# Kernel tuning notes

Hardware: AMD Instinct MI355X
Metric: run time of the kernel (lower is better)

## Reference

```python
import jax, jax.numpy as jnp
import numpy as np
import math

DIM = 2048
NUM_HEADS = 16
HEAD_DIM = 128
SEQ = 2048
BATCH = 2
THETA = 10000.0


def _rope_freqs(seq_len, head_dim, theta=THETA):
    half = head_dim // 2
    inv = 1.0 / (theta ** (np.arange(0, half, dtype=np.float32) / half))
    t = np.arange(seq_len, dtype=np.float32)
    ang = np.outer(t, inv)  # [S, half]
    return jnp.asarray(np.cos(ang)), jnp.asarray(np.sin(ang))


def setup_inputs() -> dict:
    key = jax.random.key(0)
    ks = jax.random.split(key, 5)
    s = 1.0 / math.sqrt(DIM)
    cos, sin = _rope_freqs(SEQ, HEAD_DIM)
    return {
        "x": jax.random.normal(ks[0], (BATCH, SEQ, DIM), dtype=jnp.float32),
        "wq": jax.random.normal(ks[1], (DIM, NUM_HEADS * HEAD_DIM), dtype=jnp.float32) * s,
        "wk": jax.random.normal(ks[2], (DIM, NUM_HEADS * HEAD_DIM), dtype=jnp.float32) * s,
        "wv": jax.random.normal(ks[3], (DIM, NUM_HEADS * HEAD_DIM), dtype=jnp.float32) * s,
        "wo": jax.random.normal(ks[4], (NUM_HEADS * HEAD_DIM, DIM), dtype=jnp.float32) * s,
        "freqs_cos": cos,
        "freqs_sin": sin,
    }


def _apply_rope(x, cos, sin):
    # x: [B, S, H, Hd]; cos/sin: [S, Hd//2]
    B, S, H, Hd = x.shape
    xr = x.astype(jnp.float32).reshape(B, S, H, Hd // 2, 2)
    x0, x1 = xr[..., 0], xr[..., 1]
    c = cos[:S][None, :, None, :]
    sn = sin[:S][None, :, None, :]
    o0 = x0 * c - x1 * sn
    o1 = x0 * sn + x1 * c
    return jnp.stack([o0, o1], axis=-1).reshape(B, S, H, Hd)


def reference(x, wq, wk, wv, wo, freqs_cos, freqs_sin):
    B, S, D = x.shape
    H, Hd = NUM_HEADS, HEAD_DIM
    q = (x @ wq).reshape(B, S, H, Hd)
    k = (x @ wk).reshape(B, S, H, Hd)
    v = (x @ wv).reshape(B, S, H, Hd)
    q = _apply_rope(q, freqs_cos, freqs_sin)
    k = _apply_rope(k, freqs_cos, freqs_sin)
    # [B, H, S, S] causal attention scores
    scores = jnp.einsum("bqhd,bkhd->bhqk", q, k) / math.sqrt(Hd)
    causal = jnp.tril(jnp.ones((S, S), dtype=bool))
    scores = jnp.where(causal[None, None], scores, -jnp.inf)
    probs = jax.nn.softmax(scores.astype(jnp.float32), axis=-1)
    o = jnp.einsum("bhqk,bkhd->bqhd", probs, v).reshape(B, S, H * Hd)
    return o @ wo
```

## Files before the change

### kernel.cpp

```cpp
#include <hip/hip_runtime.h>
#include <hip/hip_bf16.h>

typedef __bf16 bf16;
typedef __attribute__((ext_vector_type(8))) __bf16 bf16x8;
typedef __attribute__((ext_vector_type(4))) __bf16 bf16x4;
typedef __attribute__((ext_vector_type(4))) float  f32x4;

typedef const void __attribute__((address_space(1)))* gas_t;
typedef void __attribute__((address_space(3)))* las_t;

__device__ __forceinline__ void gload16(const void* g, void* l) {
  __builtin_amdgcn_global_load_lds((gas_t)g, (las_t)l, 16, 0, 0);
}
__device__ __forceinline__ f32x4 mfma16(bf16x8 a, bf16x8 b, f32x4 c) {
  return __builtin_amdgcn_mfma_f32_16x16x32_bf16(a, b, c, 0, 0, 0);
}
#define BARRIER() do { asm volatile("" ::: "memory"); \
  __builtin_amdgcn_s_barrier(); asm volatile("" ::: "memory"); } while (0)

constexpr int SEQL = 2048;
constexpr int DM   = 2048;
constexpr int HD   = 128;
constexpr int MR   = 4096;

__global__ __launch_bounds__(256) void cvt_x(const float* __restrict__ x,
                                             bf16* __restrict__ xb) {
  const size_t i = ((size_t)blockIdx.x * 256 + threadIdx.x) * 4;
  const f32x4 v = *reinterpret_cast<const f32x4*>(x + i);
  bf16x4 o;
  #pragma unroll
  for (int j = 0; j < 4; ++j) o[j] = (bf16)v[j];
  *reinterpret_cast<bf16x4*>(xb + i) = o;
}

__global__ __launch_bounds__(256) void transpose_w(
    const float* __restrict__ w0, const float* __restrict__ w1,
    const float* __restrict__ w2, const float* __restrict__ w3,
    bf16* __restrict__ wqkvt, bf16* __restrict__ wot) {
  const int z = blockIdx.z;
  const float* src = (z == 0) ? w0 : (z == 1) ? w1 : (z == 2) ? w2 : w3;
  bf16* dst = (z < 3) ? (wqkvt + (size_t)z * DM * DM) : wot;
  __shared__ float tile[32][33];
  const int tx = threadIdx.x, ty = threadIdx.y;
  const int x0 = blockIdx.x * 32, y0 = blockIdx.y * 32;
  #pragma unroll
  for (int i = 0; i < 4; ++i)
    tile[ty + 8 * i][tx] = src[(size_t)(y0 + ty + 8 * i) * DM + x0 + tx];
  __syncthreads();
  #pragma unroll
  for (int i = 0; i < 4; ++i)
    dst[(size_t)(x0 + ty + 8 * i) * DM + y0 + tx] = (bf16)tile[tx][ty + 8 * i];
}

__global__ __launch_bounds__(256) void rope_k(bf16* __restrict__ Q,
                                              bf16* __restrict__ Kk,
                                              const float* __restrict__ fc,
                                              const float* __restrict__ fs) {
  bf16* X = blockIdx.y ? Kk : Q;
  const size_t tid = (size_t)blockIdx.x * 256 + threadIdx.x;
  const size_t e0 = tid * 8;
  const int col = (int)(e0 & (DM - 1));
  const int row = (int)(e0 >> 11);
  const int s   = row & (SEQL - 1);
  const int p0  = (col & (HD - 1)) >> 1;
  bf16x8 v = *reinterpret_cast<bf16x8*>(X + e0);
  const f32x4 c  = *reinterpret_cast<const f32x4*>(fc + (size_t)s * 64 + p0);
  const f32x4 sn = *reinterpret_cast<const f32x4*>(fs + (size_t)s * 64 + p0);
  #pragma unroll
  for (int j = 0; j < 4; ++j) {
    const float x0 = (float)v[2 * j], x1 = (float)v[2 * j + 1];
    v[2 * j]     = (bf16)(x0 * c[j] - x1 * sn[j]);
    v[2 * j + 1] = (bf16)(x0 * sn[j] + x1 * c[j]);
  }
  *reinterpret_cast<bf16x8*>(X + e0) = v;
}

#define LDA4(DST, BASE, ROWOFF)                                                \
  {                                                                            \
    const char* ap_ = (BASE) + ((ROWOFF) + lo) * 128;                          \
    DST[0] = *(const bf16x8*)(ap_ + su0);                                      \
    DST[1] = *(const bf16x8*)(ap_ + su1);                                      \
    DST[2] = *(const bf16x8*)(ap_ + 2048 + su0);                               \
    DST[3] = *(const bf16x8*)(ap_ + 2048 + su1);                               \
  }
#define MFMAQ(Q, AR)                                                           \
  {                                                                            \
    __builtin_amdgcn_s_setprio(1);                                             \
    _Pragma("unroll")                                                          \
    for (int nf = 0; nf < 4; ++nf) {                                           \
      acc[2 * (Q)][nf]     = mfma16(AR[0], bfr[nf][0], acc[2 * (Q)][nf]);      \
      acc[2 * (Q)][nf]     = mfma16(AR[1], bfr[nf][1], acc[2 * (Q)][nf]);      \
      acc[2 * (Q) + 1][nf] = mfma16(AR[2], bfr[nf][0], acc[2 * (Q) + 1][nf]);  \
      acc[2 * (Q) + 1][nf] = mfma16(AR[3], bfr[nf][1], acc[2 * (Q) + 1][nf]);  \
    }                                                                          \
    __builtin_amdgcn_s_setprio(0);                                             \
  }

__global__ __launch_bounds__(512, 2) void gemm8(
    const bf16* __restrict__ A, const bf16* __restrict__ Bt,
    bf16* __restrict__ Cb, const int M, const int N, const int K) {
  __shared__ __attribute__((aligned(16))) char lds[131072];
  const int t = threadIdx.x;
  const int wid = t >> 6, lane = t & 63, lo = lane & 15, hi = lane >> 4;
  const int wm = wid >> 2, wn = wid & 3;

  const int bid = blockIdx.x;
  const int xcd = bid & 7, idx = bid >> 3;
  const int my = (xcd << 1) | (idx & 1);
  const int nxz = idx >> 1;
  const int nx = nxz & 7, z = nxz >> 3;
  const int m0 = my * 256, n0 = nx * 256;
  const bf16* Bt_ = Bt + (size_t)z * N * K;
  bf16* Cb_ = Cb + (size_t)z * M * N;

  const int urow  = (wid << 3) + (lane >> 3);
  const int uunit = (lane & 7) ^ ((lane >> 3) & 7);
  const bf16* gA = A   + (size_t)(m0 + urow) * K + uunit * 8;
  const bf16* gB = Bt_ + (size_t)(n0 + urow) * K + uunit * 8;
  char* lw = lds + wid * 1024;
  const int NT = K >> 6;

  auto stg = [&](const bf16* gbase, int buf, int op, int h, int kt) {
    const bf16* g = gbase + (size_t)(h * 128) * K + kt * 64;
    char* l = lw + (((buf << 1) | op) * 2 + h) * 16384;
    gload16(g, l);
    gload16(g + (size_t)64 * K, l + 8192);
  };
  auto stB0 = [&](int k2) { stg(gB, k2 & 1, 1, 0, k2); };
  auto stB1 = [&](int k2) { stg(gB, k2 & 1, 1, 1, k2); };
  auto stA0 = [&](int k2) { stg(gA, k2 & 1, 0, 0, k2); };
  auto stA1 = [&](int k2) { stg(gA, k2 & 1, 0, 1, k2); };

  f32x4 acc[8][4];
  #pragma unroll
  for (int i = 0; i < 8; ++i)
    #pragma unroll
    for (int j = 0; j < 4; ++j) acc[i][j] = (f32x4){0.f, 0.f, 0.f, 0.f};

  const int su0 = (hi ^ (lo & 7)) * 16;
  const int su1 = ((4 + hi) ^ (lo & 7)) * 16;

  stB0(0); stB1(0); stA0(0); stA1(0);
  stB0(1); stB1(1); stA0(1); stA1(1);
  asm volatile("s_waitcnt vmcnt(8)" ::: "memory");
  BARRIER();

  bf16x8 aP0[4], aP1[4];
  LDA4(aP0, lds + wm * 16384, 0);

  #pragma unroll 1
  for (int kt = 0; kt < NT; ++kt) {
    const int bc = kt & 1;
    const char* aB = lds + (bc * 4 + wm) * 16384;
    const char* bB = lds + ((bc * 2 + 1) * 2 + (wn >> 1)) * 16384;
    const char* aN = lds + (((kt + 1) & 1) * 4 + wm) * 16384;
    bf16x8 bfr[4][2];
    {
      const char* bp = bB + ((wn & 1) * 64 + lo) * 128;
      #pragma unroll
      for (int nf = 0; nf < 4; ++nf) {
        bfr[nf][0] = *(const bf16x8*)(bp + nf * 2048 + su0);
        bfr[nf][1] = *(const bf16x8*)(bp + nf * 2048 + su1);
      }
    }
    LDA4(aP1, aB, 32);
    BARRIER();
    MFMAQ(0, aP0)
    BARRIER();
    LDA4(aP0, aB, 64);
    if (kt + 2 < NT) stB0(kt + 2);
    BARRIER();
    MFMAQ(1, aP1)
    BARRIER();
    LDA4(aP1, aB, 96);
    if (kt + 2 < NT) stB1(kt + 2);
    BARRIER();
    MFMAQ(2, aP0)
    BARRIER();
    if (kt + 2 < NT)      { asm volatile("s_waitcnt vmcnt(4)" ::: "memory"); }
    else if (kt + 1 < NT) { asm volatile("s_waitcnt vmcnt(0)" ::: "memory"); }
    BARRIER();
    if (kt + 1 < NT) LDA4(aP0, aN, 0);
    if (kt + 2 < NT) { stA0(kt + 2); stA1(kt + 2); }
    MFMAQ(3, aP1)
    BARRIER();
  }

  #pragma unroll
  for (int mf = 0; mf < 8; ++mf)
    #pragma unroll
    for (int nf = 0; nf < 4; ++nf)
      #pragma unroll
      for (int r = 0; r < 4; ++r) {
        const size_t row = m0 + wm * 128 + mf * 16 + hi * 4 + r;
        const size_t col = n0 + wn * 64 + nf * 16 + lo;
        Cb_[row * N + col] = (bf16)acc[mf][nf][r];
      }
}

__global__ __launch_bounds__(256) void gemm_bt_f32(
    const bf16* __restrict__ A, const bf16* __restrict__ Bt,
    float* __restrict__ Cf, const int M, const int N, const int K) {
  const int t = threadIdx.x;
  const int wid = t >> 6, lane = t & 63, lo = lane & 15, hi = lane >> 4;
  const int m0 = blockIdx.y * 128, n0 = blockIdx.x * 128;
  __shared__ bf16 As[128 * 32];
  __shared__ bf16 Bs[128 * 32];
  const int wr = wid >> 1, wc = wid & 1;
  const f32x4 zero4 = {0.f, 0.f, 0.f, 0.f};
  f32x4 acc[4][4];
  #pragma unroll
  for (int i = 0; i < 4; ++i)
    #pragma unroll
    for (int j = 0; j < 4; ++j) acc[i][j] = zero4;

  const int r_a = t >> 2;
  const int ul  = ((t & 3) ^ (r_a & 3)) * 8;
  const bf16* gA0 = A  + (size_t)(m0 + r_a) * K + ul;
  const bf16* gB0 = Bt + (size_t)(n0 + r_a) * K + ul;
  char* lA = (char*)As + wid * 1024;
  char* lB = (char*)Bs + wid * 1024;

  const int ru = (hi ^ (lo & 3)) * 8;

  for (int k0 = 0; k0 < K; k0 += 32) {
    gload16(gA0 + k0, lA);
    gload16(gA0 + (size_t)64 * K + k0, lA + 4096);
    gload16(gB0 + k0, lB);
    gload16(gB0 + (size_t)64 * K + k0, lB + 4096);
    __syncthreads();
    bf16x8 af[4], bb[4];
    #pragma unroll
    for (int i = 0; i < 4; ++i)
      af[i] = *reinterpret_cast<const bf16x8*>(As + (wr * 64 + i * 16 + lo) * 32 + ru);
    #pragma unroll
    for (int i = 0; i < 4; ++i)
      bb[i] = *reinterpret_cast<const bf16x8*>(Bs + (wc * 64 + i * 16 + lo) * 32 + ru);
    #pragma unroll
    for (int mi = 0; mi < 4; ++mi)
      #pragma unroll
      for (int ni = 0; ni < 4; ++ni)
        acc[mi][ni] = mfma16(af[mi], bb[ni], acc[mi][ni]);
    __syncthreads();
  }
  #pragma unroll
  for (int mi = 0; mi < 4; ++mi)
    #pragma unroll
    for (int ni = 0; ni < 4; ++ni)
      #pragma unroll
      for (int r = 0; r < 4; ++r) {
        const size_t row = m0 + wr * 64 + mi * 16 + hi * 4 + r;
        const size_t col = n0 + wc * 64 + ni * 16 + lo;
        Cf[row * N + col] = acc[mi][ni][r];
      }
}

__global__ __launch_bounds__(512) void flash_fwd(
    const bf16* __restrict__ Qg, const bf16* __restrict__ Kg,
    const bf16* __restrict__ Vg, bf16* __restrict__ Og) {
  const int t = threadIdx.x;
  const int wid = t >> 6, lane = t & 63, lo = lane & 15, hi = lane >> 4;
  const int h  = blockIdx.y;
  const int b  = blockIdx.z;

  __shared__ bf16 Ks[64 * 128];
  __shared__ bf16 Vt[128 * 64];
  __shared__ bf16 Ps[8][16 * 64];

  const size_t hoff = (size_t)b * SEQL * DM + (size_t)h * HD;
  const float SCALE_LOG2 = 0.12751743f;

  const int krow = t >> 4;
  const int kul  = ((t & 15) ^ (krow & 15)) * 8;
  const int vd0  = (t & 31) * 4;
  const int vg   = (t >> 5) & 15;
  char* myP = (char*)(Ps[wid]);
  const f32x4 zero4 = {0.f, 0.f, 0.f, 0.f};

  #pragma unroll 1
  for (int pass = 0; pass < 2; ++pass) {
    const int q0 = (pass ? (15 - (int)blockIdx.x) : (int)blockIdx.x) * 128;

    bf16x8 qf[4];
    {
      const bf16* qrow = Qg + hoff + (size_t)(q0 + wid * 16 + lo) * DM;
      #pragma unroll
      for (int kc = 0; kc < 4; ++kc)
        qf[kc] = *reinterpret_cast<const bf16x8*>(qrow + kc * 32 + hi * 8);
    }

    f32x4 acc[8];
    #pragma unroll
    for (int i = 0; i < 8; ++i) acc[i] = zero4;
    float m_run = -1e30f, l_run = 0.f;

    const int ntiles = q0 / 64 + 2;
    #pragma unroll 1
    for (int it = 0; it < ntiles; ++it) {
      const int kv0 = it * 64;
      {
        const bf16* gK = Kg + hoff + (size_t)(kv0 + krow) * DM + kul;
        char* lK = (char*)Ks + wid * 1024;
        gload16(gK, lK);
        gload16(gK + (size_t)32 * DM, lK + 8192);
      }
      {
        const bf16* gV = Vg + hoff + (size_t)(kv0 + vg * 4) * DM + vd0;
        bf16x4 ld[4];
        #pragma unroll
        for (int e = 0; e < 4; ++e)
          ld[e] = *reinterpret_cast<const bf16x4*>(gV + (size_t)e * DM);
        #pragma unroll
        for (int c = 0; c < 4; ++c) {
          const int d = vd0 + c;
          const int sw = (d ^ (d >> 3)) & 7;
          bf16x4 w;
          #pragma unroll
          for (int e = 0; e < 4; ++e) w[e] = ld[e][c];
          *reinterpret_cast<bf16x4*>(Vt + d * 64 + (((vg >> 1) ^ sw) * 8) +
                                     (vg & 1) * 4) = w;
        }
      }
      __syncthreads();

      f32x4 s[4];
      #pragma unroll
      for (int nf = 0; nf < 4; ++nf) s[nf] = zero4;
      #pragma unroll
      for (int nf = 0; nf < 4; ++nf) {
        const bf16* krp = Ks + (nf * 16 + lo) * 128;
        #pragma unroll
        for (int kc = 0; kc < 4; ++kc) {
          const bf16x8 kb = *reinterpret_cast<const bf16x8*>(krp + (((kc * 4 + hi) ^ lo) * 8));
          s[nf] = mfma16(kb, qf[kc], s[nf]);
        }
      }
      const bool boundary = (kv0 + 63 > q0 + wid * 16);
      #pragma unroll
      for (int nf = 0; nf < 4; ++nf)
        #pragma unroll
        for (int r = 0; r < 4; ++r) {
          float v = s[nf][r] * SCALE_LOG2;
          if (boundary && (kv0 + nf * 16 + hi * 4 + r > q0 + wid * 16 + lo)) v = -1e30f;
          s[nf][r] = v;
        }
      float pmax = -1e30f;
      #pragma unroll
      for (int nf = 0; nf < 4; ++nf)
        #pragma unroll
        for (int r = 0; r < 4; ++r) pmax = fmaxf(pmax, s[nf][r]);
      pmax = fmaxf(pmax, __shfl_xor(pmax, 16, 64));
      pmax = fmaxf(pmax, __shfl_xor(pmax, 32, 64));
      float mnew = m_run;
      if (!__all(pmax <= m_run)) {
        mnew = fmaxf(m_run, pmax);
        const float fctr = exp2f(m_run - mnew);
        m_run = mnew;
        l_run *= fctr;
        float fa[4];
        #pragma unroll
        for (int r = 0; r < 4; ++r) fa[r] = __shfl(fctr, hi * 4 + r, 64);
        #pragma unroll
        for (int i = 0; i < 8; ++i)
          #pragma unroll
          for (int r = 0; r < 4; ++r) acc[i][r] *= fa[r];
      }
      float sum = 0.f;
      #pragma unroll
      for (int nf = 0; nf < 4; ++nf)
        #pragma unroll
        for (int r = 0; r < 4; ++r) {
          const float p = exp2f(s[nf][r] - mnew);
          s[nf][r] = p;
          sum += p;
        }
      sum += __shfl_xor(sum, 16, 64);
      sum += __shfl_xor(sum, 32, 64);
      l_run += sum;
      #pragma unroll
      for (int nf = 0; nf < 4; ++nf) {
        bf16x4 w;
        #pragma unroll
        for (int r = 0; r < 4; ++r) w[r] = (bf16)s[nf][r];
        *reinterpret_cast<bf16x4*>(myP + lo * 128 +
            (((nf * 2 + (hi >> 1)) ^ (lo & 7)) * 16) + (hi & 1) * 8) = w;
      }
      bf16x8 pa[2];
      #pragma unroll
      for (int kc = 0; kc < 2; ++kc)
        pa[kc] = *reinterpret_cast<const bf16x8*>(myP + lo * 128 +
            (((kc * 4 + hi) ^ (lo & 7)) * 16));
      #pragma unroll
      for (int nf = 0; nf < 8; ++nf) {
        const int d = nf * 16 + lo;
        const int sw = (d ^ (d >> 3)) & 7;
        const bf16* vrp = Vt + d * 64;
        #pragma unroll
        for (int kc = 0; kc < 2; ++kc) {
          const bf16x8 bv = *reinterpret_cast<const bf16x8*>(vrp + (((kc * 4 + hi) ^ sw) * 8));
          acc[nf] = mfma16(pa[kc], bv, acc[nf]);
        }
      }
      __syncthreads();
    }

    const float linv = 1.f / l_run;
    float la[4];
    #pragma unroll
    for (int r = 0; r < 4; ++r) la[r] = __shfl(linv, hi * 4 + r, 64);
    #pragma unroll
    for (int nf = 0; nf < 8; ++nf)
      #pragma unroll
      for (int r = 0; r < 4; ++r) {
        const size_t row = q0 + wid * 16 + hi * 4 + r;
        Og[hoff + row * DM + nf * 16 + lo] = (bf16)(acc[nf][r] * la[r]);
      }
  }
}

extern "C" void kernel_launch(void* const* d_in, const int* in_sizes, int n_in,
                              void* d_out, int out_size, void* d_ws, size_t ws_size,
                              hipStream_t stream) {
  const float* x  = (const float*)d_in[0];
  const float* wq = (const float*)d_in[1];
  const float* wk = (const float*)d_in[2];
  const float* wv = (const float*)d_in[3];
  const float* wo = (const float*)d_in[4];
  const float* fc = (const float*)d_in[5];
  const float* fs = (const float*)d_in[6];
  float* out = (float*)d_out;

  char* ws = (char*)d_ws;
  bf16* xb    = (bf16*)ws;
  bf16* wqkvt = (bf16*)(ws + (16ull << 20));
  bf16* wot   = (bf16*)(ws + (40ull << 20));
  bf16* qkv   = (bf16*)(ws + (48ull << 20));
  bf16* Qb = qkv;
  bf16* Kb = qkv + (size_t)MR * DM;
  bf16* Vb = qkv + 2 * (size_t)MR * DM;

  cvt_x<<<8192, 256, 0, stream>>>(x, xb);
  transpose_w<<<dim3(64, 64, 4), dim3(32, 8), 0, stream>>>(wq, wk, wv, wo, wqkvt, wot);
  gemm8<<<384, 512, 0, stream>>>(xb, wqkvt, qkv, MR, DM, DM);
  rope_k<<<dim3(4096, 2), 256, 0, stream>>>(Qb, Kb, fc, fs);
  flash_fwd<<<dim3(8, 16, 2), 512, 0, stream>>>(Qb, Kb, Vb, xb );
  gemm_bt_f32<<<dim3(16, 32), 256, 0, stream>>>(xb, wot, out, MR, DM, DM);
}
```

Measured before the change: 419.0 us.

## Reuse pipelined GEMM for output projection and widen flash-attention per-wave query tile

Templates the pipelined 256x256 gemm8 kernel on output type so the output projection can use it with fp32 stores, replacing the simple single-buffered gemm_bt_f32. Flash attention now launches 256-thread blocks, each wave handling 32 query rows (two 16-row subtiles). Each K/V tile loaded into LDS is therefore reused across twice as many MFMAs per wave. The two-pass per-block load balancing is dropped in favour of reversing query-tile order by batch index. Risks include only 128 blocks for the output GEMM, which underfills the CUs, plus higher register pressure and less even causal work per block in attention.

```diff
diff --git a/kernel.cpp b/kernel.cpp
--- a/kernel.cpp
+++ b/kernel.cpp
@@ -96,9 +96,10 @@
     __builtin_amdgcn_s_setprio(0);                                             \
   }
 
+template <bool F32OUT>
 __global__ __launch_bounds__(512, 2) void gemm8(
     const bf16* __restrict__ A, const bf16* __restrict__ Bt,
-    bf16* __restrict__ Cb, const int M, const int N, const int K) {
+    void* __restrict__ Cv, const int M, const int N, const int K) {
   __shared__ __attribute__((aligned(16))) char lds[131072];
   const int t = threadIdx.x;
   const int wid = t >> 6, lane = t & 63, lo = lane & 15, hi = lane >> 4;
@@ -111,7 +112,6 @@
   const int nx = nxz & 7, z = nxz >> 3;
   const int m0 = my * 256, n0 = nx * 256;
   const bf16* Bt_ = Bt + (size_t)z * N * K;
-  bf16* Cb_ = Cb + (size_t)z * M * N;
 
   const int urow  = (wid << 3) + (lane >> 3);
   const int uunit = (lane & 7) ^ ((lane >> 3) & 7);
@@ -194,217 +194,176 @@
       for (int r = 0; r < 4; ++r) {
         const size_t row = m0 + wm * 128 + mf * 16 + hi * 4 + r;
         const size_t col = n0 + wn * 64 + nf * 16 + lo;
-        Cb_[row * N + col] = (bf16)acc[mf][nf][r];
-      }
-}
-
-__global__ __launch_bounds__(256) void gemm_bt_f32(
-    const bf16* __restrict__ A, const bf16* __restrict__ Bt,
-    float* __restrict__ Cf, const int M, const int N, const int K) {
-  const int t = threadIdx.x;
-  const int wid = t >> 6, lane = t & 63, lo = lane & 15, hi = lane >> 4;
-  const int m0 = blockIdx.y * 128, n0 = blockIdx.x * 128;
-  __shared__ bf16 As[128 * 32];
-  __shared__ bf16 Bs[128 * 32];
-  const int wr = wid >> 1, wc = wid & 1;
-  const f32x4 zero4 = {0.f, 0.f, 0.f, 0.f};
-  f32x4 acc[4][4];
-  #pragma unroll
-  for (int i = 0; i < 4; ++i)
-    #pragma unroll
-    for (int j = 0; j < 4; ++j) acc[i][j] = zero4;
-
-  const int r_a = t >> 2;
-  const int ul  = ((t & 3) ^ (r_a & 3)) * 8;
-  const bf16* gA0 = A  + (size_t)(m0 + r_a) * K + ul;
-  const bf16* gB0 = Bt + (size_t)(n0 + r_a) * K + ul;
-  char* lA = (char*)As + wid * 1024;
-  char* lB = (char*)Bs + wid * 1024;
-
-  const int ru = (hi ^ (lo & 3)) * 8;
-
-  for (int k0 = 0; k0 < K; k0 += 32) {
-    gload16(gA0 + k0, lA);
-    gload16(gA0 + (size_t)64 * K + k0, lA + 4096);
-    gload16(gB0 + k0, lB);
-    gload16(gB0 + (size_t)64 * K + k0, lB + 4096);
-    __syncthreads();
-    bf16x8 af[4], bb[4];
-    #pragma unroll
-    for (int i = 0; i < 4; ++i)
-      af[i] = *reinterpret_cast<const bf16x8*>(As + (wr * 64 + i * 16 + lo) * 32 + ru);
-    #pragma unroll
-    for (int i = 0; i < 4; ++i)
-      bb[i] = *reinterpret_cast<const bf16x8*>(Bs + (wc * 64 + i * 16 + lo) * 32 + ru);
-    #pragma unroll
-    for (int mi = 0; mi < 4; ++mi)
-      #pragma unroll
-      for (int ni = 0; ni < 4; ++ni)
-        acc[mi][ni] = mfma16(af[mi], bb[ni], acc[mi][ni]);
-    __syncthreads();
-  }
-  #pragma unroll
-  for (int mi = 0; mi < 4; ++mi)
-    #pragma unroll
-    for (int ni = 0; ni < 4; ++ni)
-      #pragma unroll
-      for (int r = 0; r < 4; ++r) {
-        const size_t row = m0 + wr * 64 + mi * 16 + hi * 4 + r;
-        const size_t col = n0 + wc * 64 + ni * 16 + lo;
-        Cf[row * N + col] = acc[mi][ni][r];
-      }
-}
-
-__global__ __launch_bounds__(512) void flash_fwd(
+        if (F32OUT)
+          ((float*)Cv)[((size_t)z * M * N) + row * N + col] = acc[mf][nf][r];
+        else
+          ((bf16*)Cv)[((size_t)z * M * N) + row * N + col] = (bf16)acc[mf][nf][r];
+      }
+}
+
+__global__ __launch_bounds__(256, 2) void flash_fwd(
     const bf16* __restrict__ Qg, const bf16* __restrict__ Kg,
     const bf16* __restrict__ Vg, bf16* __restrict__ Og) {
   const int t = threadIdx.x;
   const int wid = t >> 6, lane = t & 63, lo = lane & 15, hi = lane >> 4;
   const int h  = blockIdx.y;
   const int b  = blockIdx.z;
+  const int qi = b ? (15 - (int)blockIdx.x) : (int)blockIdx.x;
+  const int q0 = qi * 128;
 
   __shared__ bf16 Ks[64 * 128];
   __shared__ bf16 Vt[128 * 64];
-  __shared__ bf16 Ps[8][16 * 64];
+  __shared__ bf16 Ps[4][32 * 64];
 
   const size_t hoff = (size_t)b * SEQL * DM + (size_t)h * HD;
   const float SCALE_LOG2 = 0.12751743f;
 
   const int krow = t >> 4;
-  const int kul  = ((t & 15) ^ (krow & 15)) * 8;
+  const int kul  = ((t & 15) ^ krow) * 8;
   const int vd0  = (t & 31) * 4;
-  const int vg   = (t >> 5) & 15;
+  const int vg   = t >> 5;
   char* myP = (char*)(Ps[wid]);
   const f32x4 zero4 = {0.f, 0.f, 0.f, 0.f};
 
+  bf16x8 qf[2][4];
+  #pragma unroll
+  for (int s = 0; s < 2; ++s) {
+    const bf16* qrow = Qg + hoff + (size_t)(q0 + wid * 32 + s * 16 + lo) * DM;
+    #pragma unroll
+    for (int kc = 0; kc < 4; ++kc)
+      qf[s][kc] = *reinterpret_cast<const bf16x8*>(qrow + kc * 32 + hi * 8);
+  }
+
+  f32x4 acc[2][8];
+  #pragma unroll
+  for (int s = 0; s < 2; ++s)
+    #pragma unroll
+    for (int i = 0; i < 8; ++i) acc[s][i] = zero4;
+  float m_run[2] = {-1e30f, -1e30f}, l_run[2] = {0.f, 0.f};
+
+  const int ntiles = q0 / 64 + 2;
   #pragma unroll 1
-  for (int pass = 0; pass < 2; ++pass) {
-    const int q0 = (pass ? (15 - (int)blockIdx.x) : (int)blockIdx.x) * 128;
-
-    bf16x8 qf[4];
+  for (int it = 0; it < ntiles; ++it) {
+    const int kv0 = it * 64;
     {
-      const bf16* qrow = Qg + hoff + (size_t)(q0 + wid * 16 + lo) * DM;
-      #pragma unroll
-      for (int kc = 0; kc < 4; ++kc)
-        qf[kc] = *reinterpret_cast<const bf16x8*>(qrow + kc * 32 + hi * 8);
-    }
-
-    f32x4 acc[8];
-    #pragma unroll
-    for (int i = 0; i < 8; ++i) acc[i] = zero4;
-    float m_run = -1e30f, l_run = 0.f;
-
-    const int ntiles = q0 / 64 + 2;
-    #pragma unroll 1
-    for (int it = 0; it < ntiles; ++it) {
-      const int kv0 = it * 64;
-      {
-        const bf16* gK = Kg + hoff + (size_t)(kv0 + krow) * DM + kul;
-        char* lK = (char*)Ks + wid * 1024;
-        gload16(gK, lK);
-        gload16(gK + (size_t)32 * DM, lK + 8192);
-      }
-      {
-        const bf16* gV = Vg + hoff + (size_t)(kv0 + vg * 4) * DM + vd0;
-        bf16x4 ld[4];
-        #pragma unroll
-        for (int e = 0; e < 4; ++e)
-          ld[e] = *reinterpret_cast<const bf16x4*>(gV + (size_t)e * DM);
-        #pragma unroll
-        for (int c = 0; c < 4; ++c) {
-          const int d = vd0 + c;
-          const int sw = (d ^ (d >> 3)) & 7;
-          bf16x4 w;
-          #pragma unroll
-          for (int e = 0; e < 4; ++e) w[e] = ld[e][c];
-          *reinterpret_cast<bf16x4*>(Vt + d * 64 + (((vg >> 1) ^ sw) * 8) +
-                                     (vg & 1) * 4) = w;
-        }
-      }
-      __syncthreads();
-
-      f32x4 s[4];
-      #pragma unroll
-      for (int nf = 0; nf < 4; ++nf) s[nf] = zero4;
-      #pragma unroll
-      for (int nf = 0; nf < 4; ++nf) {
-        const bf16* krp = Ks + (nf * 16 + lo) * 128;
-        #pragma unroll
-        for (int kc = 0; kc < 4; ++kc) {
-          const bf16x8 kb = *reinterpret_cast<const bf16x8*>(krp + (((kc * 4 + hi) ^ lo) * 8));
-          s[nf] = mfma16(kb, qf[kc], s[nf]);
-        }
-      }
-      const bool boundary = (kv0 + 63 > q0 + wid * 16);
+      const bf16* gK = Kg + hoff + (size_t)(kv0 + krow) * DM + kul;
+      char* lK = (char*)Ks + wid * 1024;
+      #pragma unroll
+      for (int j = 0; j < 4; ++j)
+        gload16(gK + (size_t)j * 16 * DM, lK + j * 4096);
+    }
+    {
+      const bf16* gV = Vg + hoff + (size_t)kv0 * DM + vd0;
+      bf16x4 ld[8];
+      #pragma unroll
+      for (int e = 0; e < 8; ++e)
+        ld[e] = *reinterpret_cast<const bf16x4*>(gV + (size_t)(vg * 8 + e) * DM);
+      #pragma unroll
+      for (int c = 0; c < 4; ++c) {
+        const int d = vd0 + c;
+        const int sw = (d ^ (d >> 3)) & 7;
+        bf16x8 pk;
+        #pragma unroll
+        for (int e = 0; e < 8; ++e) pk[e] = ld[e][c];
+        *reinterpret_cast<bf16x8*>(Vt + d * 64 + ((vg ^ sw) * 8)) = pk;
+      }
+    }
+    __syncthreads();
+
+    f32x4 sv[2][4];
+    #pragma unroll
+    for (int s = 0; s < 2; ++s)
+      #pragma unroll
+      for (int nf = 0; nf < 4; ++nf) sv[s][nf] = zero4;
+    #pragma unroll
+    for (int nf = 0; nf < 4; ++nf) {
+      const bf16* krp = Ks + (nf * 16 + lo) * 128;
+      #pragma unroll
+      for (int kc = 0; kc < 4; ++kc) {
+        const bf16x8 kb = *reinterpret_cast<const bf16x8*>(krp + (((kc * 4 + hi) ^ lo) * 8));
+        sv[0][nf] = mfma16(kb, qf[0][kc], sv[0][nf]);
+        sv[1][nf] = mfma16(kb, qf[1][kc], sv[1][nf]);
+      }
+    }
+    #pragma unroll
+    for (int s = 0; s < 2; ++s) {
+      const int qrow = q0 + wid * 32 + s * 16 + lo;
+      const bool boundary = (kv0 + 63 > q0 + wid * 32 + s * 16);
       #pragma unroll
       for (int nf = 0; nf < 4; ++nf)
         #pragma unroll
         for (int r = 0; r < 4; ++r) {
-          float v = s[nf][r] * SCALE_LOG2;
-          if (boundary && (kv0 + nf * 16 + hi * 4 + r > q0 + wid * 16 + lo)) v = -1e30f;
-          s[nf][r] = v;
+          float v = sv[s][nf][r] * SCALE_LOG2;
+          if (boundary && (kv0 + nf * 16 + hi * 4 + r > qrow)) v = -1e30f;
+          sv[s][nf][r] = v;
         }
       float pmax = -1e30f;
       #pragma unroll
       for (int nf = 0; nf < 4; ++nf)
         #pragma unroll
-        for (int r = 0; r < 4; ++r) pmax = fmaxf(pmax, s[nf][r]);
+        for (int r = 0; r < 4; ++r) pmax = fmaxf(pmax, sv[s][nf][r]);
       pmax = fmaxf(pmax, __shfl_xor(pmax, 16, 64));
       pmax = fmaxf(pmax, __shfl_xor(pmax, 32, 64));
-      float mnew = m_run;
-      if (!__all(pmax <= m_run)) {
-        mnew = fmaxf(m_run, pmax);
-        const float fctr = exp2f(m_run - mnew);
-        m_run = mnew;
-        l_run *= fctr;
+      float mnew = m_run[s];
+      if (!__all(pmax <= m_run[s])) {
+        mnew = fmaxf(m_run[s], pmax);
+        const float fctr = exp2f(m_run[s] - mnew);
+        m_run[s] = mnew;
+        l_run[s] *= fctr;
         float fa[4];
         #pragma unroll
         for (int r = 0; r < 4; ++r) fa[r] = __shfl(fctr, hi * 4 + r, 64);
         #pragma unroll
         for (int i = 0; i < 8; ++i)
           #pragma unroll
-          for (int r = 0; r < 4; ++r) acc[i][r] *= fa[r];
+          for (int r = 0; r < 4; ++r) acc[s][i][r] *= fa[r];
       }
       float sum = 0.f;
       #pragma unroll
       for (int nf = 0; nf < 4; ++nf)
         #pragma unroll
         for (int r = 0; r < 4; ++r) {
-          const float p = exp2f(s[nf][r] - mnew);
-          s[nf][r] = p;
+          const float p = exp2f(sv[s][nf][r] - mnew);
+          sv[s][nf][r] = p;
           sum += p;
         }
       sum += __shfl_xor(sum, 16, 64);
       sum += __shfl_xor(sum, 32, 64);
-      l_run += sum;
+      l_run[s] += sum;
       #pragma unroll
       for (int nf = 0; nf < 4; ++nf) {
         bf16x4 w;
         #pragma unroll
-        for (int r = 0; r < 4; ++r) w[r] = (bf16)s[nf][r];
-        *reinterpret_cast<bf16x4*>(myP + lo * 128 +
+        for (int r = 0; r < 4; ++r) w[r] = (bf16)sv[s][nf][r];
+        *reinterpret_cast<bf16x4*>(myP + (s * 16 + lo) * 128 +
             (((nf * 2 + (hi >> 1)) ^ (lo & 7)) * 16) + (hi & 1) * 8) = w;
       }
-      bf16x8 pa[2];
+    }
+    bf16x8 pa[2][2];
+    #pragma unroll
+    for (int s = 0; s < 2; ++s)
       #pragma unroll
       for (int kc = 0; kc < 2; ++kc)
-        pa[kc] = *reinterpret_cast<const bf16x8*>(myP + lo * 128 +
+        pa[s][kc] = *reinterpret_cast<const bf16x8*>(myP + (s * 16 + lo) * 128 +
             (((kc * 4 + hi) ^ (lo & 7)) * 16));
-      #pragma unroll
-      for (int nf = 0; nf < 8; ++nf) {
-        const int d = nf * 16 + lo;
-        const int sw = (d ^ (d >> 3)) & 7;
-        const bf16* vrp = Vt + d * 64;
-        #pragma unroll
-        for (int kc = 0; kc < 2; ++kc) {
-          const bf16x8 bv = *reinterpret_cast<const bf16x8*>(vrp + (((kc * 4 + hi) ^ sw) * 8));
-          acc[nf] = mfma16(pa[kc], bv, acc[nf]);
-        }
-      }
-      __syncthreads();
-    }
-
-    const float linv = 1.f / l_run;
+    #pragma unroll
+    for (int nf = 0; nf < 8; ++nf) {
+      const int d = nf * 16 + lo;
+      const int sw = (d ^ (d >> 3)) & 7;
+      const bf16* vrp = Vt + d * 64;
+      #pragma unroll
+      for (int kc = 0; kc < 2; ++kc) {
+        const bf16x8 bv = *reinterpret_cast<const bf16x8*>(vrp + (((kc * 4 + hi) ^ sw) * 8));
+        acc[0][nf] = mfma16(pa[0][kc], bv, acc[0][nf]);
+        acc[1][nf] = mfma16(pa[1][kc], bv, acc[1][nf]);
+      }
+    }
+    __syncthreads();
+  }
+
+  #pragma unroll
+  for (int s = 0; s < 2; ++s) {
+    const float linv = 1.f / l_run[s];
     float la[4];
     #pragma unroll
     for (int r = 0; r < 4; ++r) la[r] = __shfl(linv, hi * 4 + r, 64);
@@ -412,8 +371,8 @@
     for (int nf = 0; nf < 8; ++nf)
       #pragma unroll
       for (int r = 0; r < 4; ++r) {
-        const size_t row = q0 + wid * 16 + hi * 4 + r;
-        Og[hoff + row * DM + nf * 16 + lo] = (bf16)(acc[nf][r] * la[r]);
+        const size_t row = q0 + wid * 32 + s * 16 + hi * 4 + r;
+        Og[hoff + row * DM + nf * 16 + lo] = (bf16)(acc[s][nf][r] * la[r]);
       }
   }
 }
@@ -441,8 +400,8 @@
 
   cvt_x<<<8192, 256, 0, stream>>>(x, xb);
   transpose_w<<<dim3(64, 64, 4), dim3(32, 8), 0, stream>>>(wq, wk, wv, wo, wqkvt, wot);
-  gemm8<<<384, 512, 0, stream>>>(xb, wqkvt, qkv, MR, DM, DM);
+  gemm8<false><<<384, 512, 0, stream>>>(xb, wqkvt, (void*)qkv, MR, DM, DM);
   rope_k<<<dim3(4096, 2), 256, 0, stream>>>(Qb, Kb, fc, fs);
-  flash_fwd<<<dim3(8, 16, 2), 512, 0, stream>>>(Qb, Kb, Vb, xb );
-  gemm_bt_f32<<<dim3(16, 32), 256, 0, stream>>>(xb, wot, out, MR, DM, DM);
-}
+  flash_fwd<<<dim3(16, 16, 2), 256, 0, stream>>>(Qb, Kb, Vb, xb );
+  gemm8<true><<<128, 512, 0, stream>>>(xb, wot, (void*)out, MR, DM, DM);
+}
```

Measured after the change: 433.9 us. 3.6% more time.
